# Optimization experiments

Measured on AMD Instinct MI355X. Metric: run time of the kernel, lower is better.

## Reference

```python
import jax, jax.numpy as jnp
import numpy as np


def setup_inputs() -> dict:
    key = jax.random.key(0)
    ks = jax.random.split(key, 7)
    N, d, dout = 4096, 16, 16
    return {
        "nodes": jax.random.normal(ks[0], (N, d), dtype=jnp.float32),
        "W_bil": jax.random.normal(ks[1], (dout, d, d), dtype=jnp.float32) * 0.1,
        "b_bil": jax.random.normal(ks[2], (dout,), dtype=jnp.float32) * 0.1,
        "W2": jax.random.normal(ks[3], (16, 16), dtype=jnp.float32) * 0.25,
        "b2": jax.random.normal(ks[4], (16,), dtype=jnp.float32) * 0.1,
        "W3": jax.random.normal(ks[5], (16, 16), dtype=jnp.float32) * 0.25,
        "b3": jax.random.normal(ks[6], (16,), dtype=jnp.float32) * 0.1,
        "num_batches": 4,
    }


def reference(nodes, W_bil, b_bil, W2, b2, W3, b3, num_batches):
    # nodes: [N, d]; num_batches B equal-sized events -> [B, M, d]
    N, d = nodes.shape
    B = int(num_batches)
    M = N // B
    X = nodes.reshape(B, M, d)

    # Bilinear over all ordered pairs: e[b,i,j,k] = x_i^T W_k x_j + b_k
    T = jnp.einsum('bid,kde->bike', X, W_bil)          # [B, M, K, d]
    E = jnp.einsum('bike,bje->bijk', T, X) + b_bil     # [B, M, M, K]

    # Linear layers (y = x @ W^T + b), applied pointwise over edges
    E = jnp.einsum('bijk,ok->bijo', E, W2) + b2
    E = jnp.einsum('bijk,ok->bijo', E, W3) + b3

    # Drop self-edges (i == j) with static index gather (M is static)
    off_i, off_j = np.where(~np.eye(M, dtype=bool))
    edge_features = E[:, off_i, off_j, :].reshape(B * M * (M - 1), -1)
    return edge_features
```

## Files before the change

kernel.cpp:

```cpp
#include <hip/hip_runtime.h>
#include <hip/hip_bf16.h>

typedef __attribute__((ext_vector_type(8))) short short8;
typedef __attribute__((ext_vector_type(4))) float f32x4;


__global__ void k_prep(const float* __restrict__ nodes,
                       const float* __restrict__ W_bil,
                       const float* __restrict__ b_bil,
                       const float* __restrict__ W2,
                       const float* __restrict__ b2,
                       const float* __restrict__ W3,
                       const float* __restrict__ b3,
                       float* __restrict__ Weff,
                       float* __restrict__ beff,
                       __hip_bfloat16* __restrict__ Xb,
                       int N)
{
    const int p = blockIdx.x;
    const int t = threadIdx.x;

    __shared__ float wc[16];
    if (t < 16) {
        float s = 0.f;
        #pragma unroll
        for (int o = 0; o < 16; ++o) s += W3[p * 16 + o] * W2[o * 16 + t];
        wc[t] = s;
    }
    __syncthreads();

    {
        const int d = t >> 4, e = t & 15;
        float s = 0.f;
        #pragma unroll
        for (int k = 0; k < 16; ++k) s += wc[k] * W_bil[(k * 16 + d) * 16 + e];
        Weff[(p * 16 + d) * 16 + e] = s;
    }

    if (p == 0 && t < 16) {
        float acc = b3[t];
        #pragma unroll
        for (int o = 0; o < 16; ++o) acc += W3[t * 16 + o] * b2[o];
        #pragma unroll
        for (int k = 0; k < 16; ++k) {
            float wck = 0.f;
            #pragma unroll
            for (int o = 0; o < 16; ++o) wck += W3[t * 16 + o] * W2[o * 16 + k];
            acc += wck * b_bil[k];
        }
        beff[t] = acc;
    }

    {
        const int n = p * 256 + t;
        if (n < N) {
            const float* src = nodes + (size_t)n * 16;
            __hip_bfloat16* dst = Xb + (size_t)n * 32;
            #pragma unroll
            for (int e = 0; e < 16; ++e) dst[e] = __float2bfloat16(src[e]);
            #pragma unroll
            for (int e = 16; e < 32; ++e) dst[e] = __float2bfloat16(0.f);
        }
    }
}

__global__ __launch_bounds__(256) void k_main(
    const float* __restrict__ nodes,
    const float* __restrict__ Weff,
    const __hip_bfloat16* __restrict__ Xb,
    const float* __restrict__ beff,
    float* __restrict__ out,
    int M)
{
    const int blk  = blockIdx.x;
    const int il   = blk % M;
    const int bM   = blk - il;
    const int t    = threadIdx.x;

    __shared__ float xr[16];
    __shared__ __hip_bfloat16 Us[16 * 32];
    if (t < 16) xr[t] = nodes[(size_t)blk * 16 + t];
    __syncthreads();
    {
        const int p = t >> 4, e = t & 15;
        float s = 0.f;
        #pragma unroll
        for (int d = 0; d < 16; ++d) s += xr[d] * Weff[(p * 16 + d) * 16 + e];
        Us[p * 32 + e]      = __float2bfloat16(s);
        Us[p * 32 + 16 + e] = __float2bfloat16(0.f);
    }
    __syncthreads();

    const int w    = t >> 6;
    const int lane = t & 63;
    const int q    = lane >> 4;
    const int r16  = lane & 15;

    const short8 a = *reinterpret_cast<const short8*>(
        reinterpret_cast<const unsigned short*>(Us) + r16 * 32 + q * 8);

    f32x4 cinit;
    {
        const float4 bv = *reinterpret_cast<const float4*>(beff + q * 4);
        cinit = f32x4{bv.x, bv.y, bv.z, bv.w};
    }

    const unsigned short* Xu = reinterpret_cast<const unsigned short*>(Xb);
    const size_t xbase = (size_t)bM * 32;
    float* outb = out + (size_t)blk * (M - 1) * 16;

    const int ntiles = M >> 4;
    #pragma unroll 4
    for (int jt = w; jt < ntiles; jt += 4) {
        const int j = jt * 16 + r16;
        const short8 bfr = *reinterpret_cast<const short8*>(
            Xu + xbase + (size_t)j * 32 + q * 8);
        f32x4 acc = __builtin_amdgcn_mfma_f32_16x16x32_bf16(a, bfr, cinit, 0, 0, 0);
        if (j != il) {
            const int jj = j - (j > il);
            f32x4* dst = reinterpret_cast<f32x4*>(outb + (size_t)jj * 16 + q * 4);
            __builtin_nontemporal_store(acc, dst);
        }
    }
}

extern "C" void kernel_launch(void* const* d_in, const int* in_sizes, int n_in,
                              void* d_out, int out_size, void* d_ws, size_t ws_size,
                              hipStream_t stream)
{
    const float* nodes = (const float*)d_in[0];
    const float* W_bil = (const float*)d_in[1];
    const float* b_bil = (const float*)d_in[2];
    const float* W2    = (const float*)d_in[3];
    const float* b2    = (const float*)d_in[4];
    const float* W3    = (const float*)d_in[5];
    const float* b3    = (const float*)d_in[6];
    const int N = in_sizes[0] / 16;
    const int M = out_size / (16 * N) + 1;

    char* ws = (char*)d_ws;
    float*          Weff = (float*)(ws);
    float*          beff = (float*)(ws + 16384);
    __hip_bfloat16* Xb   = (__hip_bfloat16*)(ws + 16448);
    float* out = (float*)d_out;

    k_prep<<<16, 256, 0, stream>>>(nodes, W_bil, b_bil, W2, b2, W3, b3,
                                   Weff, beff, Xb, N);
    k_main<<<N, 256, 0, stream>>>(nodes, Weff, Xb, beff, out, M);
}
```

Baseline: 289.8 us.

## Precompute per-row U in separate kernel and assign one row per wavefront

The per-row projection U = x_i^T Weff moves out of the main kernel into a new kernel that writes bf16 U rows to workspace. The main kernel now gives each wavefront its own output row i, so a block covers four rows and loops over all j tiles, with no shared memory or barriers. Nontemporal stores are replaced by plain stores. This removes the per-block prologue and syncs, but adds an extra kernel launch and a global round trip for U.

```diff
diff --git a/kernel.cpp b/kernel.cpp
--- a/kernel.cpp
+++ b/kernel.cpp
@@ -64,40 +64,47 @@
     }
 }
 
+__global__ void k_u(const float* __restrict__ nodes,
+                    const float* __restrict__ Weff,
+                    __hip_bfloat16* __restrict__ U)
+{
+    const int i = blockIdx.x;
+    const int t = threadIdx.x;
+
+    __shared__ float xr[16];
+    if (t < 16) xr[t] = nodes[(size_t)i * 16 + t];
+    __syncthreads();
+
+    const int p = t >> 4, e = t & 15;
+    float s = 0.f;
+    #pragma unroll
+    for (int d = 0; d < 16; ++d) s += xr[d] * Weff[(p * 16 + d) * 16 + e];
+
+    __hip_bfloat16* row = U + (size_t)i * 512;
+    row[p * 32 + e]      = __float2bfloat16(s);
+    row[p * 32 + 16 + e] = __float2bfloat16(0.f);
+}
+
 __global__ __launch_bounds__(256) void k_main(
-    const float* __restrict__ nodes,
-    const float* __restrict__ Weff,
+    const __hip_bfloat16* __restrict__ U,
     const __hip_bfloat16* __restrict__ Xb,
     const float* __restrict__ beff,
     float* __restrict__ out,
     int M)
 {
-    const int blk  = blockIdx.x;
-    const int il   = blk % M;
-    const int bM   = blk - il;
     const int t    = threadIdx.x;
-
-    __shared__ float xr[16];
-    __shared__ __hip_bfloat16 Us[16 * 32];
-    if (t < 16) xr[t] = nodes[(size_t)blk * 16 + t];
-    __syncthreads();
-    {
-        const int p = t >> 4, e = t & 15;
-        float s = 0.f;
-        #pragma unroll
-        for (int d = 0; d < 16; ++d) s += xr[d] * Weff[(p * 16 + d) * 16 + e];
-        Us[p * 32 + e]      = __float2bfloat16(s);
-        Us[p * 32 + 16 + e] = __float2bfloat16(0.f);
-    }
-    __syncthreads();
-
     const int w    = t >> 6;
     const int lane = t & 63;
     const int q    = lane >> 4;
     const int r16  = lane & 15;
 
+    const int blk = blockIdx.x * 4 + w;
+    const int il  = blk % M;
+    const int bM  = blk - il;
+
+    const unsigned short* Uu = reinterpret_cast<const unsigned short*>(U);
     const short8 a = *reinterpret_cast<const short8*>(
-        reinterpret_cast<const unsigned short*>(Us) + r16 * 32 + q * 8);
+        Uu + (size_t)blk * 512 + r16 * 32 + q * 8);
 
     f32x4 cinit;
     {
@@ -111,15 +118,15 @@
 
     const int ntiles = M >> 4;
     #pragma unroll 4
-    for (int jt = w; jt < ntiles; jt += 4) {
+    for (int jt = 0; jt < ntiles; ++jt) {
         const int j = jt * 16 + r16;
         const short8 bfr = *reinterpret_cast<const short8*>(
             Xu + xbase + (size_t)j * 32 + q * 8);
-        f32x4 acc = __builtin_amdgcn_mfma_f32_16x16x32_bf16(a, bfr, cinit, 0, 0, 0);
+        const f32x4 acc = __builtin_amdgcn_mfma_f32_16x16x32_bf16(a, bfr, cinit, 0, 0, 0);
         if (j != il) {
             const int jj = j - (j > il);
             f32x4* dst = reinterpret_cast<f32x4*>(outb + (size_t)jj * 16 + q * 4);
-            __builtin_nontemporal_store(acc, dst);
+            *dst = acc;
         }
     }
 }
@@ -142,9 +149,11 @@
     float*          Weff = (float*)(ws);
     float*          beff = (float*)(ws + 16384);
     __hip_bfloat16* Xb   = (__hip_bfloat16*)(ws + 16448);
+    __hip_bfloat16* U    = (__hip_bfloat16*)(ws + 16448 + (size_t)N * 64);
     float* out = (float*)d_out;
 
     k_prep<<<16, 256, 0, stream>>>(nodes, W_bil, b_bil, W2, b2, W3, b3,
                                    Weff, beff, Xb, N);
-    k_main<<<N, 256, 0, stream>>>(nodes, Weff, Xb, beff, out, M);
+    k_u<<<N, 256, 0, stream>>>(nodes, Weff, U);
+    k_main<<<N / 4, 256, 0, stream>>>(U, Xb, beff, out, M);
 }
```

Result: faster. 275.7 us (-4.9%).
